# Optimization experiments

Measured on AMD Instinct MI355X. Metric: run time of the kernel, lower is better.

## Reference

```python
import jax, jax.numpy as jnp
import numpy as np

B, T, C = 2, 2048, 2048
H, HKV, D = 16, 4, 128
R = 64  # rope_dim = head_dim * rotary_pct


def setup_inputs() -> dict:
    key = jax.random.key(0)
    ks = jax.random.split(key, 8)
    s = 0.02
    return {
        "x": jax.random.normal(ks[0], (B, T, C), jnp.float32),
        "cos": jnp.cos(jax.random.normal(ks[1], (T, R), jnp.float32)),
        "sin": jnp.sin(jax.random.normal(ks[2], (T, R), jnp.float32)),
        "Wq": jax.random.normal(ks[3], (C, C), jnp.float32) * s,
        "Wk": jax.random.normal(ks[4], (C, HKV * D), jnp.float32) * s,
        "Wv": jax.random.normal(ks[5], (C, HKV * D), jnp.float32) * s,
        "Wo": jax.random.normal(ks[6], (C, C), jnp.float32) * s,
        "gate": jax.random.normal(ks[7], (H,), jnp.float32) * 0.1 - 3.0,
    }


def _rotate_half(t):
    t1, t2 = t[..., : t.shape[-1] // 2], t[..., t.shape[-1] // 2:]
    return jnp.concatenate([-t2, t1], axis=-1)


def reference(x, cos, sin, Wq, Wk, Wv, Wo, gate):
    # projections -> (B, heads, T, D)
    q = (x @ Wq).reshape(B, T, H, D).transpose(0, 2, 1, 3)
    k = (x @ Wk).reshape(B, T, HKV, D).transpose(0, 2, 1, 3)
    v = (x @ Wv).reshape(B, T, HKV, D).transpose(0, 2, 1, 3)

    # partial RoPE on first R dims; cos/sin (T,R) broadcast over (B,h,T,R)
    q_r = q[..., :R] * cos + _rotate_half(q[..., :R]) * sin
    k_r = k[..., :R] * cos + _rotate_half(k[..., :R]) * sin
    q = jnp.concatenate([q_r, q[..., R:]], axis=-1)
    k = jnp.concatenate([k_r, k[..., R:]], axis=-1)

    # GQA: repeat_interleave kv heads to match H
    rep = H // HKV
    k = jnp.repeat(k, rep, axis=1)
    v = jnp.repeat(v, rep, axis=1)

    scale = D ** -0.5
    att = jnp.einsum("bhtd,bhsd->bhts", q, k) * scale  # (B,H,T,T)
    causal = jnp.tril(jnp.ones((T, T), bool))
    att = jnp.where(causal, att, -jnp.inf)
    att = jax.nn.softmax(att, axis=-1)

    # post-softmax learned per-head threshold gate
    thr = jax.nn.sigmoid(gate)[None, :, None, None]
    att = att * (att >= thr).astype(att.dtype)

    y = jnp.einsum("bhts,bhsd->bhtd", att, v)
    y = y.transpose(0, 2, 1, 3).reshape(B, T, C)
    return y @ Wo
```

## Files before the change

kernel.cpp:

```cpp
#include <hip/hip_runtime.h>
#include <stdint.h>

#define Bdim 2
#define Tdim 2048
#define Cdim 2048
#define Hdim 16
#define HKVdim 4
#define KVdim 512
#define KT 32

typedef __attribute__((ext_vector_type(8))) short bf16x8;
typedef __attribute__((ext_vector_type(4))) float f32x4;

#define GLOAD16(gp, lp) __builtin_amdgcn_global_load_lds( \
    (const __attribute__((address_space(1))) void*)(gp),  \
    (__attribute__((address_space(3))) void*)(lp), 16, 0, 0)

__device__ __forceinline__ unsigned short f2bf(float f) {
  union { float f; unsigned u; } a; a.f = f;
  unsigned u = a.u + 0x7FFFu + ((a.u >> 16) & 1u);
  return (unsigned short)(u >> 16);
}
__device__ __forceinline__ float bf2f(unsigned short h) {
  union { float f; unsigned u; } a; a.u = ((unsigned)h) << 16;
  return a.f;
}

__global__ void split_x_kernel(const float* __restrict__ x, unsigned short* __restrict__ hi,
                               unsigned short* __restrict__ lo, int n4) {
  int i = blockIdx.x * blockDim.x + threadIdx.x;
  int stride = gridDim.x * blockDim.x;
  const float4* x4 = (const float4*)x;
  ushort4* h4 = (ushort4*)hi;
  ushort4* l4 = (ushort4*)lo;
  for (; i < n4; i += stride) {
    float4 f = x4[i];
    ushort4 h, l;
    h.x = f2bf(f.x); l.x = f2bf(f.x - bf2f(h.x));
    h.y = f2bf(f.y); l.y = f2bf(f.y - bf2f(h.y));
    h.z = f2bf(f.z); l.z = f2bf(f.z - bf2f(h.z));
    h.w = f2bf(f.w); l.w = f2bf(f.w - bf2f(h.w));
    h4[i] = h; l4[i] = l;
  }
}

__global__ void transpose_split_kernel(const float* __restrict__ in, unsigned short* __restrict__ hi,
                                       unsigned short* __restrict__ lo, int K, int N) {
  __shared__ float tile[32][33];
  int k0 = blockIdx.x * 32, n0 = blockIdx.y * 32;
  int tx = threadIdx.x, ty = threadIdx.y;
#pragma unroll
  for (int i = 0; i < 32; i += 8)
    tile[ty + i][tx] = in[(size_t)(k0 + ty + i) * N + n0 + tx];
  __syncthreads();
#pragma unroll
  for (int i = 0; i < 32; i += 8) {
    float f = tile[tx][ty + i];
    size_t o = (size_t)(n0 + ty + i) * K + k0 + tx;
    unsigned short hb = f2bf(f);
    hi[o] = hb;
    if (lo) lo[o] = f2bf(f - bf2f(hb));
  }
}

__global__ __launch_bounds__(256) void qkv_gemm_kernel(
    const unsigned short* __restrict__ xhi, const unsigned short* __restrict__ xlo,
    const unsigned short* __restrict__ WqThi, const unsigned short* __restrict__ WqTlo,
    const unsigned short* __restrict__ WkThi, const unsigned short* __restrict__ WkTlo,
    const unsigned short* __restrict__ WvThi,
    const float* __restrict__ cs, const float* __restrict__ sn,
    unsigned short* __restrict__ qhi, unsigned short* __restrict__ qlo,
    unsigned short* __restrict__ khi, unsigned short* __restrict__ klo,
    unsigned short* __restrict__ vun)
{
  __shared__ alignas(16) unsigned short sAh[2][128 * 32];
  __shared__ alignas(16) unsigned short sAl[2][128 * 32];
  __shared__ alignas(16) unsigned short sBh[2][128 * 32];
  __shared__ alignas(16) unsigned short sBl[2][128 * 32];
  const int K = 2048;
  int tid = threadIdx.x;
  int wid = tid >> 6, lane = tid & 63;
  int bm = blockIdx.x, bn = blockIdx.y;
  int wr = wid >> 1, wc = wid & 1;
  int ln15 = lane & 15;
  int jsw = (((lane >> 4) ^ ((ln15 >> 1) & 3)) * 8);
  int srow = lane >> 2;
  int scol = (((lane & 3) ^ ((lane >> 3) & 3)) * 8);
  bool three = bn < 20;

  const unsigned short *Bh, *Bl = WqTlo;
  int brow;
  if (bn < 16)      { Bh = WqThi; Bl = WqTlo; brow = bn * 128; }
  else if (bn < 20) { Bh = WkThi; Bl = WkTlo; brow = (bn - 16) * 128; }
  else              { Bh = WvThi;             brow = (bn - 20) * 128; }

  f32x4 acc[4][4];
#pragma unroll
  for (int m = 0; m < 4; ++m)
#pragma unroll
    for (int n = 0; n < 4; ++n)
      acc[m][n] = f32x4{0.f, 0.f, 0.f, 0.f};

  const unsigned short* a0 = xhi + (size_t)(bm * 128 + wid * 32 + srow) * K + scol;
  const unsigned short* a1 = xlo + (size_t)(bm * 128 + wid * 32 + srow) * K + scol;
  const unsigned short* b0 = Bh + (size_t)(brow + wid * 32 + srow) * K + scol;
  const unsigned short* b1 = Bl + (size_t)(brow + wid * 32 + srow) * K + scol;
  int wlds = wid * 32 * 32;

  int nk = K >> 5;
  if (three) {
    auto stage3 = [&](int buf, int kt) {
      const unsigned short* ak = a0 + kt * 32;
      const unsigned short* alk = a1 + kt * 32;
      const unsigned short* bk = b0 + kt * 32;
      const unsigned short* blk = b1 + kt * 32;
      GLOAD16(ak,          &sAh[buf][wlds]);
      GLOAD16(ak + 16 * K, &sAh[buf][wlds + 16 * 32]);
      GLOAD16(alk,          &sAl[buf][wlds]);
      GLOAD16(alk + 16 * K, &sAl[buf][wlds + 16 * 32]);
      GLOAD16(bk,          &sBh[buf][wlds]);
      GLOAD16(bk + 16 * K, &sBh[buf][wlds + 16 * 32]);
      GLOAD16(blk,          &sBl[buf][wlds]);
      GLOAD16(blk + 16 * K, &sBl[buf][wlds + 16 * 32]);
    };
    stage3(0, 0);
    __syncthreads();
    int buf = 0;
    for (int kt = 0; kt < nk; ++kt) {
      bf16x8 afh[4], afl[4], bfh[4], bfl[4];
#pragma unroll
      for (int m = 0; m < 4; ++m) {
        afh[m] = *(const bf16x8*)&sAh[buf][(wr * 64 + m * 16 + ln15) * 32 + jsw];
        afl[m] = *(const bf16x8*)&sAl[buf][(wr * 64 + m * 16 + ln15) * 32 + jsw];
      }
#pragma unroll
      for (int n = 0; n < 4; ++n) {
        bfh[n] = *(const bf16x8*)&sBh[buf][(wc * 64 + n * 16 + ln15) * 32 + jsw];
        bfl[n] = *(const bf16x8*)&sBl[buf][(wc * 64 + n * 16 + ln15) * 32 + jsw];
      }
      if (kt + 1 < nk) stage3(buf ^ 1, kt + 1);
      __builtin_amdgcn_s_setprio(1);
#pragma unroll
      for (int m = 0; m < 4; ++m)
#pragma unroll
        for (int n = 0; n < 4; ++n)
          acc[m][n] = __builtin_amdgcn_mfma_f32_16x16x32_bf16(afh[m], bfh[n], acc[m][n], 0, 0, 0);
#pragma unroll
      for (int m = 0; m < 4; ++m)
#pragma unroll
        for (int n = 0; n < 4; ++n)
          acc[m][n] = __builtin_amdgcn_mfma_f32_16x16x32_bf16(afl[m], bfh[n], acc[m][n], 0, 0, 0);
#pragma unroll
      for (int m = 0; m < 4; ++m)
#pragma unroll
        for (int n = 0; n < 4; ++n)
          acc[m][n] = __builtin_amdgcn_mfma_f32_16x16x32_bf16(afh[m], bfl[n], acc[m][n], 0, 0, 0);
      __builtin_amdgcn_s_setprio(0);
      __syncthreads();
      buf ^= 1;
    }
  } else {
    auto stage1 = [&](int buf, int kt) {
      const unsigned short* ak = a0 + kt * 32;
      const unsigned short* bk = b0 + kt * 32;
      GLOAD16(ak,          &sAh[buf][wlds]);
      GLOAD16(ak + 16 * K, &sAh[buf][wlds + 16 * 32]);
      GLOAD16(bk,          &sBh[buf][wlds]);
      GLOAD16(bk + 16 * K, &sBh[buf][wlds + 16 * 32]);
    };
    stage1(0, 0);
    __syncthreads();
    int buf = 0;
    for (int kt = 0; kt < nk; ++kt) {
      bf16x8 afh[4], bfh[4];
#pragma unroll
      for (int m = 0; m < 4; ++m)
        afh[m] = *(const bf16x8*)&sAh[buf][(wr * 64 + m * 16 + ln15) * 32 + jsw];
#pragma unroll
      for (int n = 0; n < 4; ++n)
        bfh[n] = *(const bf16x8*)&sBh[buf][(wc * 64 + n * 16 + ln15) * 32 + jsw];
      if (kt + 1 < nk) stage1(buf ^ 1, kt + 1);
      __builtin_amdgcn_s_setprio(1);
#pragma unroll
      for (int m = 0; m < 4; ++m)
#pragma unroll
        for (int n = 0; n < 4; ++n)
          acc[m][n] = __builtin_amdgcn_mfma_f32_16x16x32_bf16(afh[m], bfh[n], acc[m][n], 0, 0, 0);
      __builtin_amdgcn_s_setprio(0);
      __syncthreads();
      buf ^= 1;
    }
  }

  int orow0 = bm * 128 + wr * 64 + (lane >> 4) * 4;
  if (bn < 20) {
    int nh = (bn < 16) ? Hdim : HKVdim;
    int h  = (bn < 16) ? bn : bn - 16;
    unsigned short* oph = (bn < 16) ? qhi : khi;
    unsigned short* opl = (bn < 16) ? qlo : klo;
#pragma unroll
    for (int m = 0; m < 4; ++m)
#pragma unroll
      for (int r = 0; r < 4; ++r) {
        int row = orow0 + m * 16 + r;
        int t = row & (Tdim - 1), b = row >> 11;
        size_t obase = (((size_t)(b * nh + h)) * Tdim + t) * 128;
#pragma unroll
        for (int n = 0; n < 4; ++n) {
          int d = wc * 64 + n * 16 + ln15;
          float o;
          if (wc == 0) {
            float c = cs[t * 64 + d], s = sn[t * 64 + d];
            o = (n < 2) ? (acc[m][n][r] * c - acc[m][n + 2][r] * s)
                        : (acc[m][n][r] * c + acc[m][n - 2][r] * s);
          } else o = acc[m][n][r];
          unsigned short hb = f2bf(o);
          oph[obase + d] = hb;
          opl[obase + d] = f2bf(o - bf2f(hb));
        }
      }
  } else {
    int g = bn - 20;
#pragma unroll
    for (int m = 0; m < 4; ++m)
#pragma unroll
      for (int r = 0; r < 4; ++r) {
        int row = orow0 + m * 16 + r;
        int t = row & (Tdim - 1), b = row >> 11;
        size_t obase = (((size_t)(b * HKVdim + g)) * Tdim + t) * 128;
#pragma unroll
        for (int n = 0; n < 4; ++n)
          vun[obase + wc * 64 + n * 16 + ln15] = f2bf(acc[m][n][r]);
      }
  }
}

__global__ __launch_bounds__(256) void gemm_wo_kernel(
    const unsigned short* __restrict__ A, const unsigned short* __restrict__ Bt,
    float* __restrict__ C)
{
  __shared__ alignas(16) unsigned short sA[2][128 * 32];
  __shared__ alignas(16) unsigned short sB[2][128 * 32];
  const int K = 2048, ldc = 2048;
  int tid = threadIdx.x;
  int wid = tid >> 6, lane = tid & 63;
  int bm = blockIdx.x, bn = blockIdx.y;
  int wr = wid >> 1, wc = wid & 1;
  int ln15 = lane & 15;
  int jsw = (((lane >> 4) ^ ((ln15 >> 1) & 3)) * 8);
  int srow = lane >> 2;
  int scol = (((lane & 3) ^ ((lane >> 3) & 3)) * 8);

  f32x4 acc[4][4];
#pragma unroll
  for (int m = 0; m < 4; ++m)
#pragma unroll
    for (int n = 0; n < 4; ++n)
      acc[m][n] = f32x4{0.f, 0.f, 0.f, 0.f};

  const unsigned short* a0 = A + (size_t)(bm * 128 + wid * 32 + srow) * K + scol;
  const unsigned short* b0 = Bt + (size_t)(bn * 128 + wid * 32 + srow) * K + scol;
  int wlds = wid * 32 * 32;

  auto stage = [&](int buf, int kt) {
    const unsigned short* ak = a0 + kt * 32;
    const unsigned short* bk = b0 + kt * 32;
    GLOAD16(ak,          &sA[buf][wlds]);
    GLOAD16(ak + 16 * K, &sA[buf][wlds + 16 * 32]);
    GLOAD16(bk,          &sB[buf][wlds]);
    GLOAD16(bk + 16 * K, &sB[buf][wlds + 16 * 32]);
  };
  int nk = K >> 5;
  stage(0, 0);
  __syncthreads();
  int buf = 0;
  for (int kt = 0; kt < nk; ++kt) {
    bf16x8 af[4], bfv[4];
#pragma unroll
    for (int m = 0; m < 4; ++m)
      af[m] = *(const bf16x8*)&sA[buf][(wr * 64 + m * 16 + ln15) * 32 + jsw];
#pragma unroll
    for (int n = 0; n < 4; ++n)
      bfv[n] = *(const bf16x8*)&sB[buf][(wc * 64 + n * 16 + ln15) * 32 + jsw];
    if (kt + 1 < nk) stage(buf ^ 1, kt + 1);
    __builtin_amdgcn_s_setprio(1);
#pragma unroll
    for (int m = 0; m < 4; ++m)
#pragma unroll
      for (int n = 0; n < 4; ++n)
        acc[m][n] = __builtin_amdgcn_mfma_f32_16x16x32_bf16(af[m], bfv[n], acc[m][n], 0, 0, 0);
    __builtin_amdgcn_s_setprio(0);
    __syncthreads();
    buf ^= 1;
  }

  int orow0 = bm * 128 + wr * 64 + (lane >> 4) * 4;
  int ocol0 = bn * 128 + wc * 64 + ln15;
#pragma unroll
  for (int m = 0; m < 4; ++m)
#pragma unroll
    for (int n = 0; n < 4; ++n)
#pragma unroll
      for (int r = 0; r < 4; ++r)
        C[(size_t)(orow0 + m * 16 + r) * ldc + ocol0 + n * 16] = acc[m][n][r];
}

__global__ void transpose_v_bf16_kernel(const unsigned short* __restrict__ vsrc,
                                        unsigned short* __restrict__ vt) {
  __shared__ unsigned short tile[32][33];
  int bg = blockIdx.x;
  int t0 = blockIdx.y * 32, d0 = blockIdx.z * 32;
  int tx = threadIdx.x, ty = threadIdx.y;
#pragma unroll
  for (int i = 0; i < 32; i += 8)
    tile[ty + i][tx] = vsrc[((size_t)bg * Tdim + t0 + ty + i) * 128 + d0 + tx];
  __syncthreads();
#pragma unroll
  for (int i = 0; i < 32; i += 8)
    vt[((size_t)(bg * 128 + d0 + ty + i)) * Tdim + t0 + tx] = tile[tx][ty + i];
}

__global__ __launch_bounds__(1024, 4) void attn_kernel(
    const unsigned short* __restrict__ qhi, const unsigned short* __restrict__ qlo,
    const unsigned short* __restrict__ khi, const unsigned short* __restrict__ klo,
    const unsigned short* __restrict__ vt, const float* __restrict__ gate,
    unsigned short* __restrict__ y)
{
  __shared__ alignas(16) unsigned short sKh[2][KT * 128];
  __shared__ alignas(16) unsigned short sKl[2][KT * 128];
  __shared__ alignas(16) unsigned short sV[2][128 * KT];
  __shared__ alignas(16) unsigned short sP[16][16 * 40];
  __shared__ float sBM[16][64];

  int qb = (gridDim.x - 1) - blockIdx.x;
  int bh = blockIdx.y;
  int b = bh >> 4, h = bh & 15;
  int g = h >> 2;
  int t0 = qb * 256;
  int tid = threadIdx.x, wid = tid >> 6, lane = tid & 63;
  int ln15 = lane & 15, j16 = (lane >> 4) * 16, ro4 = (lane >> 4) * 4;
  const float cs2 = 0.08838834764831845f * 1.4426950408889634f;
  const float M2  = 8.0f * 1.4426950408889634f;

  const unsigned short* kh_base = khi + (((size_t)b * HKVdim + g) * Tdim) * 128;
  const unsigned short* kl_base = klo + (((size_t)b * HKVdim + g) * Tdim) * 128;
  const unsigned short* v_base  = vt  + (((size_t)b * HKVdim + g) * 128) * (size_t)Tdim;

  bf16x8 aqh[4], aql[4];
  {
    size_t qoff = ((((size_t)b * Hdim + h) * Tdim) + t0 + wid * 16 + ln15) * 128 + (lane >> 4) * 8;
#pragma unroll
    for (int kf = 0; kf < 4; ++kf) {
      aqh[kf] = *(const bf16x8*)(qhi + qoff + kf * 32);
      aql[kf] = *(const bf16x8*)(qlo + qoff + kf * 32);
    }
  }
  float thr = 1.f / (1.f + expf(-gate[h]));

  int nkb = (qb + 1) * 8;
  int tq_lo = t0 + wid * 16;

  auto stageK = [&](int buf, int kb) {
    if (wid < 8) {
      int o = wid * 1024 + lane * 16;
      int row = o >> 8;
      int col = (o & 255) ^ ((row & 7) << 4);
      size_t goff = ((size_t)(kb * KT + row)) * 256 + col;
      GLOAD16((const char*)kh_base + goff, (char*)sKh[buf] + wid * 1024);
      GLOAD16((const char*)kl_base + goff, (char*)sKl[buf] + wid * 1024);
    }
  };
  auto stageV = [&](int buf, int kb) {
    if (wid >= 8) {
      int o = (wid - 8) * 1024 + lane * 16;
      int row = o >> 6;
      int col = (o & 63) ^ (((row ^ (row >> 2)) & 3) << 4);
      size_t goff = (size_t)row * (Tdim * 2) + (size_t)kb * 64 + col;
      GLOAD16((const char*)v_base + goff, (char*)sV[buf] + (wid - 8) * 1024);
    }
  };
  auto qk = [&](int buf, f32x4* s) {
    __builtin_amdgcn_s_setprio(1);
#pragma unroll
    for (int nf = 0; nf < 2; ++nf) {
      f32x4 a = {0.f, 0.f, 0.f, 0.f};
      int krow = nf * 16 + ln15;
      int sw = (krow & 7) << 4;
#pragma unroll
      for (int kf = 0; kf < 4; ++kf) {
        int boff = (kf * 64 + j16) ^ sw;
        bf16x8 bh_ = *(const bf16x8*)((const char*)sKh[buf] + krow * 256 + boff);
        bf16x8 bl_ = *(const bf16x8*)((const char*)sKl[buf] + krow * 256 + boff);
        a = __builtin_amdgcn_mfma_f32_16x16x32_bf16(aqh[kf], bh_, a, 0, 0, 0);
        a = __builtin_amdgcn_mfma_f32_16x16x32_bf16(aql[kf], bh_, a, 0, 0, 0);
        a = __builtin_amdgcn_mfma_f32_16x16x32_bf16(aqh[kf], bl_, a, 0, 0, 0);
      }
      s[nf] = a;
    }
    __builtin_amdgcn_s_setprio(0);
  };

  float lloc[4];
#pragma unroll
  for (int r = 0; r < 4; ++r) lloc[r] = 0.f;

  stageK(0, 0);
  __syncthreads();
  for (int kb = 0; kb < nkb; ++kb) {
    int buf = kb & 1;
    if (kb + 1 < nkb) stageK(buf ^ 1, kb + 1);
    if (kb * KT <= tq_lo + 15) {
      f32x4 s[2];
      qk(buf, s);
      float wmax = -1e30f;
      bool full = (kb * KT + KT - 1) <= tq_lo;
      if (full) {
#pragma unroll
        for (int nf = 0; nf < 2; ++nf)
#pragma unroll
          for (int r = 0; r < 4; ++r) {
            float v = s[nf][r] * cs2;
            wmax = fmaxf(wmax, v);
            lloc[r] += __builtin_exp2f(v - M2);
          }
      } else {
#pragma unroll
        for (int nf = 0; nf < 2; ++nf) {
          int tk = kb * KT + nf * 16 + ln15;
#pragma unroll
          for (int r = 0; r < 4; ++r) {
            int tq = tq_lo + ro4 + r;
            float v = (tk <= tq) ? s[nf][r] * cs2 : -1e30f;
            wmax = fmaxf(wmax, v);
            lloc[r] += __builtin_exp2f(v - M2);
          }
        }
      }
#pragma unroll
      for (int off = 1; off < 64; off <<= 1)
        wmax = fmaxf(wmax, __shfl_xor(wmax, off));
      if (lane == 0) sBM[wid][kb] = wmax;
    }
    __syncthreads();
  }

  float lrow[4], lgate2[4];
#pragma unroll
  for (int r = 0; r < 4; ++r) {
    float l = lloc[r];
#pragma unroll
    for (int off = 1; off < 16; off <<= 1) l += __shfl_xor(l, off);
    lrow[r] = l;
    lgate2[r] = __log2f(thr * l) + M2;
  }
  float lgmin = fminf(fminf(lgate2[0], lgate2[1]), fminf(lgate2[2], lgate2[3]));
  lgmin = fminf(lgmin, __shfl_xor(lgmin, 16));
  lgmin = fminf(lgmin, __shfl_xor(lgmin, 32));

  f32x4 yacc[8];
#pragma unroll
  for (int n = 0; n < 8; ++n) yacc[n] = f32x4{0.f, 0.f, 0.f, 0.f};

  stageK(0, 0);
  stageV(0, 0);
  __syncthreads();
  for (int kb = 0; kb < nkb; ++kb) {
    int buf = kb & 1;
    if (kb + 1 < nkb) { stageK(buf ^ 1, kb + 1); stageV(buf ^ 1, kb + 1); }
    if (kb * KT <= tq_lo + 15 && sBM[wid][kb] >= lgmin) {
      f32x4 s[2];
      qk(buf, s);
      bool anyk = false;
      float pv[2][4];
      bool full = (kb * KT + KT - 1) <= tq_lo;
#pragma unroll
      for (int nf = 0; nf < 2; ++nf) {
        int tk = kb * KT + nf * 16 + ln15;
#pragma unroll
        for (int r = 0; r < 4; ++r) {
          int tq = tq_lo + ro4 + r;
          float v = s[nf][r] * cs2;
          bool keep = (full || tk <= tq) && (v >= lgate2[r]);
          float p = 0.f;
          if (keep) { p = __builtin_exp2f(v - M2); anyk = true; }
          pv[nf][r] = p;
        }
      }
      if (__any(anyk)) {
#pragma unroll
        for (int nf = 0; nf < 2; ++nf)
#pragma unroll
          for (int r = 0; r < 4; ++r)
            sP[wid][(ro4 + r) * 40 + nf * 16 + ln15] = f2bf(pv[nf][r]);
        __builtin_amdgcn_s_setprio(1);
        bf16x8 pa = *(const bf16x8*)&sP[wid][ln15 * 40 + (lane >> 4) * 8];
#pragma unroll
        for (int nf2 = 0; nf2 < 8; ++nf2) {
          int vrow = nf2 * 16 + ln15;
          int vboff = j16 ^ (((vrow ^ (vrow >> 2)) & 3) << 4);
          bf16x8 vb = *(const bf16x8*)((const char*)sV[buf] + vrow * 64 + vboff);
          yacc[nf2] = __builtin_amdgcn_mfma_f32_16x16x32_bf16(pa, vb, yacc[nf2], 0, 0, 0);
        }
        __builtin_amdgcn_s_setprio(0);
      }
    }
    __syncthreads();
  }

#pragma unroll
  for (int r = 0; r < 4; ++r) {
    int tq = t0 + wid * 16 + ro4 + r;
    float invl = 1.f / lrow[r];
    size_t base = ((size_t)(b * Tdim + tq)) * Cdim + h * 128;
#pragma unroll
    for (int nf2 = 0; nf2 < 8; ++nf2)
      y[base + nf2 * 16 + ln15] = f2bf(yacc[nf2][r] * invl);
  }
}

extern "C" void kernel_launch(void* const* d_in, const int* in_sizes, int n_in,
                              void* d_out, int out_size, void* d_ws, size_t ws_size,
                              hipStream_t stream)
{
  (void)in_sizes; (void)n_in; (void)out_size; (void)ws_size;
  const float* x    = (const float*)d_in[0];
  const float* cosT = (const float*)d_in[1];
  const float* sinT = (const float*)d_in[2];
  const float* Wq   = (const float*)d_in[3];
  const float* Wk   = (const float*)d_in[4];
  const float* Wv   = (const float*)d_in[5];
  const float* Wo   = (const float*)d_in[6];
  const float* gate = (const float*)d_in[7];
  float* out = (float*)d_out;

  char* ws = (char*)d_ws;
  size_t off = 0;
  auto alloc = [&](size_t bytes) -> char* {
    char* p = ws + off; off += (bytes + 255) & ~(size_t)255; return p;
  };
  const size_t NX = (size_t)Bdim * Tdim * Cdim;
  const size_t NK = (size_t)Bdim * Tdim * KVdim;

  unsigned short* xhi   = (unsigned short*)alloc(NX * 2);
  unsigned short* xlo   = (unsigned short*)alloc(NX * 2);
  unsigned short* WqThi = (unsigned short*)alloc((size_t)Cdim * Cdim * 2);
  unsigned short* WqTlo = (unsigned short*)alloc((size_t)Cdim * Cdim * 2);
  unsigned short* WkThi = (unsigned short*)alloc((size_t)Cdim * KVdim * 2);
  unsigned short* WkTlo = (unsigned short*)alloc((size_t)Cdim * KVdim * 2);
  unsigned short* WvThi = (unsigned short*)alloc((size_t)Cdim * KVdim * 2);
  unsigned short* WoThi = (unsigned short*)alloc((size_t)Cdim * Cdim * 2);
  unsigned short* qhi   = (unsigned short*)alloc(NX * 2);
  unsigned short* qlo   = (unsigned short*)alloc(NX * 2);
  unsigned short* khi   = (unsigned short*)alloc(NK * 2);
  unsigned short* klo   = (unsigned short*)alloc(NK * 2);
  unsigned short* vun   = (unsigned short*)alloc(NK * 2);
  unsigned short* vtr   = (unsigned short*)alloc(NK * 2);
  unsigned short* yb    = (unsigned short*)alloc(NX * 2);

  dim3 tb(32, 8);
  split_x_kernel<<<2048, 256, 0, stream>>>(x, xhi, xlo, (int)(NX >> 2));
  transpose_split_kernel<<<dim3(64, 64), tb, 0, stream>>>(Wq, WqThi, WqTlo, Cdim, Cdim);
  transpose_split_kernel<<<dim3(64, 16), tb, 0, stream>>>(Wk, WkThi, WkTlo, Cdim, KVdim);
  transpose_split_kernel<<<dim3(64, 16), tb, 0, stream>>>(Wv, WvThi, nullptr, Cdim, KVdim);
  transpose_split_kernel<<<dim3(64, 64), tb, 0, stream>>>(Wo, WoThi, nullptr, Cdim, Cdim);

  qkv_gemm_kernel<<<dim3(32, 24), 256, 0, stream>>>(
      xhi, xlo, WqThi, WqTlo, WkThi, WkTlo, WvThi,
      cosT, sinT, qhi, qlo, khi, klo, vun);
  transpose_v_bf16_kernel<<<dim3(8, 64, 4), tb, 0, stream>>>(vun, vtr);

  attn_kernel<<<dim3(8, 32), 1024, 0, stream>>>(qhi, qlo, khi, klo, vtr, gate, yb);

  gemm_wo_kernel<<<dim3(32, 16), 256, 0, stream>>>(yb, WoThi, out);
}
```

Measured before the change: 393.7 us.

## Use atomic work queue for QKV GEMM and halve attention block size

The QKV GEMM becomes a persistent kernel of 512 blocks that pull tile indices from a global atomic counter. The costlier three-pass Q and K tiles are handed out first and the cheaper single-pass V tiles last, to balance load across CUs. The attention kernel moves from 1024-thread blocks covering 256 query rows to 512-thread blocks covering 128 rows, which doubles the grid. It now single-buffers V, issuing the V load for the current key block at the start of each iteration and waiting on vmcnt just before the PV MFMAs. The trade-offs are atomic and barrier overhead per GEMM item, and V load latency that is now less hidden in attention.

```diff
diff --git a/kernel.cpp b/kernel.cpp
--- a/kernel.cpp
+++ b/kernel.cpp
@@ -15,6 +15,7 @@
 #define GLOAD16(gp, lp) __builtin_amdgcn_global_load_lds( \
     (const __attribute__((address_space(1))) void*)(gp),  \
     (__attribute__((address_space(3))) void*)(lp), 16, 0, 0)
+#define WAITV(N) asm volatile("s_waitcnt vmcnt(" #N ")" ::: "memory")
 
 __device__ __forceinline__ unsigned short f2bf(float f) {
   union { float f; unsigned u; } a; a.f = f;
@@ -71,167 +72,180 @@
     const float* __restrict__ cs, const float* __restrict__ sn,
     unsigned short* __restrict__ qhi, unsigned short* __restrict__ qlo,
     unsigned short* __restrict__ khi, unsigned short* __restrict__ klo,
-    unsigned short* __restrict__ vun)
+    unsigned short* __restrict__ vun, unsigned* __restrict__ qcnt)
 {
   __shared__ alignas(16) unsigned short sAh[2][128 * 32];
   __shared__ alignas(16) unsigned short sAl[2][128 * 32];
   __shared__ alignas(16) unsigned short sBh[2][128 * 32];
   __shared__ alignas(16) unsigned short sBl[2][128 * 32];
+  __shared__ int s_item;
   const int K = 2048;
   int tid = threadIdx.x;
   int wid = tid >> 6, lane = tid & 63;
-  int bm = blockIdx.x, bn = blockIdx.y;
   int wr = wid >> 1, wc = wid & 1;
   int ln15 = lane & 15;
   int jsw = (((lane >> 4) ^ ((ln15 >> 1) & 3)) * 8);
   int srow = lane >> 2;
   int scol = (((lane & 3) ^ ((lane >> 3) & 3)) * 8);
-  bool three = bn < 20;
-
-  const unsigned short *Bh, *Bl = WqTlo;
-  int brow;
-  if (bn < 16)      { Bh = WqThi; Bl = WqTlo; brow = bn * 128; }
-  else if (bn < 20) { Bh = WkThi; Bl = WkTlo; brow = (bn - 16) * 128; }
-  else              { Bh = WvThi;             brow = (bn - 20) * 128; }
-
-  f32x4 acc[4][4];
-#pragma unroll
-  for (int m = 0; m < 4; ++m)
-#pragma unroll
-    for (int n = 0; n < 4; ++n)
-      acc[m][n] = f32x4{0.f, 0.f, 0.f, 0.f};
-
-  const unsigned short* a0 = xhi + (size_t)(bm * 128 + wid * 32 + srow) * K + scol;
-  const unsigned short* a1 = xlo + (size_t)(bm * 128 + wid * 32 + srow) * K + scol;
-  const unsigned short* b0 = Bh + (size_t)(brow + wid * 32 + srow) * K + scol;
-  const unsigned short* b1 = Bl + (size_t)(brow + wid * 32 + srow) * K + scol;
   int wlds = wid * 32 * 32;
-
   int nk = K >> 5;
-  if (three) {
-    auto stage3 = [&](int buf, int kt) {
-      const unsigned short* ak = a0 + kt * 32;
-      const unsigned short* alk = a1 + kt * 32;
-      const unsigned short* bk = b0 + kt * 32;
-      const unsigned short* blk = b1 + kt * 32;
-      GLOAD16(ak,          &sAh[buf][wlds]);
-      GLOAD16(ak + 16 * K, &sAh[buf][wlds + 16 * 32]);
-      GLOAD16(alk,          &sAl[buf][wlds]);
-      GLOAD16(alk + 16 * K, &sAl[buf][wlds + 16 * 32]);
-      GLOAD16(bk,          &sBh[buf][wlds]);
-      GLOAD16(bk + 16 * K, &sBh[buf][wlds + 16 * 32]);
-      GLOAD16(blk,          &sBl[buf][wlds]);
-      GLOAD16(blk + 16 * K, &sBl[buf][wlds + 16 * 32]);
-    };
-    stage3(0, 0);
+
+  for (;;) {
     __syncthreads();
-    int buf = 0;
-    for (int kt = 0; kt < nk; ++kt) {
-      bf16x8 afh[4], afl[4], bfh[4], bfl[4];
-#pragma unroll
-      for (int m = 0; m < 4; ++m) {
-        afh[m] = *(const bf16x8*)&sAh[buf][(wr * 64 + m * 16 + ln15) * 32 + jsw];
-        afl[m] = *(const bf16x8*)&sAl[buf][(wr * 64 + m * 16 + ln15) * 32 + jsw];
+    if (tid == 0) s_item = (int)atomicAdd(qcnt, 1u);
+    __syncthreads();
+    int item = s_item;
+    if (item >= 768) break;
+
+    int bm, bn;
+    if (item < 512)      { bm = item >> 4; bn = item & 15; }
+    else if (item < 640) { int i = item - 512; bm = i >> 2; bn = 16 + (i & 3); }
+    else                 { int i = item - 640; bm = i >> 2; bn = 20 + (i & 3); }
+    bool three = bn < 20;
+
+    const unsigned short *Bh, *Bl = WqTlo;
+    int brow;
+    if (bn < 16)      { Bh = WqThi; Bl = WqTlo; brow = bn * 128; }
+    else if (bn < 20) { Bh = WkThi; Bl = WkTlo; brow = (bn - 16) * 128; }
+    else              { Bh = WvThi;             brow = (bn - 20) * 128; }
+
+    f32x4 acc[4][4];
+#pragma unroll
+    for (int m = 0; m < 4; ++m)
+#pragma unroll
+      for (int n = 0; n < 4; ++n)
+        acc[m][n] = f32x4{0.f, 0.f, 0.f, 0.f};
+
+    const unsigned short* a0 = xhi + (size_t)(bm * 128 + wid * 32 + srow) * K + scol;
+    const unsigned short* a1 = xlo + (size_t)(bm * 128 + wid * 32 + srow) * K + scol;
+    const unsigned short* b0 = Bh + (size_t)(brow + wid * 32 + srow) * K + scol;
+    const unsigned short* b1 = Bl + (size_t)(brow + wid * 32 + srow) * K + scol;
+
+    if (three) {
+      auto stage3 = [&](int buf, int kt) {
+        const unsigned short* ak = a0 + kt * 32;
+        const unsigned short* alk = a1 + kt * 32;
+        const unsigned short* bk = b0 + kt * 32;
+        const unsigned short* blk = b1 + kt * 32;
+        GLOAD16(ak,          &sAh[buf][wlds]);
+        GLOAD16(ak + 16 * K, &sAh[buf][wlds + 16 * 32]);
+        GLOAD16(alk,          &sAl[buf][wlds]);
+        GLOAD16(alk + 16 * K, &sAl[buf][wlds + 16 * 32]);
+        GLOAD16(bk,          &sBh[buf][wlds]);
+        GLOAD16(bk + 16 * K, &sBh[buf][wlds + 16 * 32]);
+        GLOAD16(blk,          &sBl[buf][wlds]);
+        GLOAD16(blk + 16 * K, &sBl[buf][wlds + 16 * 32]);
+      };
+      stage3(0, 0);
+      __syncthreads();
+      int buf = 0;
+      for (int kt = 0; kt < nk; ++kt) {
+        bf16x8 afh[4], afl[4], bfh[4], bfl[4];
+#pragma unroll
+        for (int m = 0; m < 4; ++m) {
+          afh[m] = *(const bf16x8*)&sAh[buf][(wr * 64 + m * 16 + ln15) * 32 + jsw];
+          afl[m] = *(const bf16x8*)&sAl[buf][(wr * 64 + m * 16 + ln15) * 32 + jsw];
+        }
+#pragma unroll
+        for (int n = 0; n < 4; ++n) {
+          bfh[n] = *(const bf16x8*)&sBh[buf][(wc * 64 + n * 16 + ln15) * 32 + jsw];
+          bfl[n] = *(const bf16x8*)&sBl[buf][(wc * 64 + n * 16 + ln15) * 32 + jsw];
+        }
+        if (kt + 1 < nk) stage3(buf ^ 1, kt + 1);
+        __builtin_amdgcn_s_setprio(1);
+#pragma unroll
+        for (int m = 0; m < 4; ++m)
+#pragma unroll
+          for (int n = 0; n < 4; ++n)
+            acc[m][n] = __builtin_amdgcn_mfma_f32_16x16x32_bf16(afh[m], bfh[n], acc[m][n], 0, 0, 0);
+#pragma unroll
+        for (int m = 0; m < 4; ++m)
+#pragma unroll
+          for (int n = 0; n < 4; ++n)
+            acc[m][n] = __builtin_amdgcn_mfma_f32_16x16x32_bf16(afl[m], bfh[n], acc[m][n], 0, 0, 0);
+#pragma unroll
+        for (int m = 0; m < 4; ++m)
+#pragma unroll
+          for (int n = 0; n < 4; ++n)
+            acc[m][n] = __builtin_amdgcn_mfma_f32_16x16x32_bf16(afh[m], bfl[n], acc[m][n], 0, 0, 0);
+        __builtin_amdgcn_s_setprio(0);
+        __syncthreads();
+        buf ^= 1;
       }
-#pragma unroll
-      for (int n = 0; n < 4; ++n) {
-        bfh[n] = *(const bf16x8*)&sBh[buf][(wc * 64 + n * 16 + ln15) * 32 + jsw];
-        bfl[n] = *(const bf16x8*)&sBl[buf][(wc * 64 + n * 16 + ln15) * 32 + jsw];
+    } else {
+      auto stage1 = [&](int buf, int kt) {
+        const unsigned short* ak = a0 + kt * 32;
+        const unsigned short* bk = b0 + kt * 32;
+        GLOAD16(ak,          &sAh[buf][wlds]);
+        GLOAD16(ak + 16 * K, &sAh[buf][wlds + 16 * 32]);
+        GLOAD16(bk,          &sBh[buf][wlds]);
+        GLOAD16(bk + 16 * K, &sBh[buf][wlds + 16 * 32]);
+      };
+      stage1(0, 0);
+      __syncthreads();
+      int buf = 0;
+      for (int kt = 0; kt < nk; ++kt) {
+        bf16x8 afh[4], bfh[4];
+#pragma unroll
+        for (int m = 0; m < 4; ++m)
+          afh[m] = *(const bf16x8*)&sAh[buf][(wr * 64 + m * 16 + ln15) * 32 + jsw];
+#pragma unroll
+        for (int n = 0; n < 4; ++n)
+          bfh[n] = *(const bf16x8*)&sBh[buf][(wc * 64 + n * 16 + ln15) * 32 + jsw];
+        if (kt + 1 < nk) stage1(buf ^ 1, kt + 1);
+        __builtin_amdgcn_s_setprio(1);
+#pragma unroll
+        for (int m = 0; m < 4; ++m)
+#pragma unroll
+          for (int n = 0; n < 4; ++n)
+            acc[m][n] = __builtin_amdgcn_mfma_f32_16x16x32_bf16(afh[m], bfh[n], acc[m][n], 0, 0, 0);
+        __builtin_amdgcn_s_setprio(0);
+        __syncthreads();
+        buf ^= 1;
       }
-      if (kt + 1 < nk) stage3(buf ^ 1, kt + 1);
-      __builtin_amdgcn_s_setprio(1);
+    }
+
+    int orow0 = bm * 128 + wr * 64 + (lane >> 4) * 4;
+    if (bn < 20) {
+      int nh = (bn < 16) ? Hdim : HKVdim;
+      int h  = (bn < 16) ? bn : bn - 16;
+      unsigned short* oph = (bn < 16) ? qhi : khi;
+      unsigned short* opl = (bn < 16) ? qlo : klo;
 #pragma unroll
       for (int m = 0; m < 4; ++m)
 #pragma unroll
-        for (int n = 0; n < 4; ++n)
-          acc[m][n] = __builtin_amdgcn_mfma_f32_16x16x32_bf16(afh[m], bfh[n], acc[m][n], 0, 0, 0);
+        for (int r = 0; r < 4; ++r) {
+          int row = orow0 + m * 16 + r;
+          int t = row & (Tdim - 1), b = row >> 11;
+          size_t obase = (((size_t)(b * nh + h)) * Tdim + t) * 128;
+#pragma unroll
+          for (int n = 0; n < 4; ++n) {
+            int d = wc * 64 + n * 16 + ln15;
+            float o;
+            if (wc == 0) {
+              float c = cs[t * 64 + d], s = sn[t * 64 + d];
+              o = (n < 2) ? (acc[m][n][r] * c - acc[m][n + 2][r] * s)
+                          : (acc[m][n][r] * c + acc[m][n - 2][r] * s);
+            } else o = acc[m][n][r];
+            unsigned short hb = f2bf(o);
+            oph[obase + d] = hb;
+            opl[obase + d] = f2bf(o - bf2f(hb));
+          }
+        }
+    } else {
+      int g = bn - 20;
 #pragma unroll
       for (int m = 0; m < 4; ++m)
 #pragma unroll
-        for (int n = 0; n < 4; ++n)
-          acc[m][n] = __builtin_amdgcn_mfma_f32_16x16x32_bf16(afl[m], bfh[n], acc[m][n], 0, 0, 0);
-#pragma unroll
-      for (int m = 0; m < 4; ++m)
-#pragma unroll
-        for (int n = 0; n < 4; ++n)
-          acc[m][n] = __builtin_amdgcn_mfma_f32_16x16x32_bf16(afh[m], bfl[n], acc[m][n], 0, 0, 0);
-      __builtin_amdgcn_s_setprio(0);
-      __syncthreads();
-      buf ^= 1;
+        for (int r = 0; r < 4; ++r) {
+          int row = orow0 + m * 16 + r;
+          int t = row & (Tdim - 1), b = row >> 11;
+          size_t obase = (((size_t)(b * HKVdim + g)) * Tdim + t) * 128;
+#pragma unroll
+          for (int n = 0; n < 4; ++n)
+            vun[obase + wc * 64 + n * 16 + ln15] = f2bf(acc[m][n][r]);
+        }
     }
-  } else {
-    auto stage1 = [&](int buf, int kt) {
-      const unsigned short* ak = a0 + kt * 32;
-      const unsigned short* bk = b0 + kt * 32;
-      GLOAD16(ak,          &sAh[buf][wlds]);
-      GLOAD16(ak + 16 * K, &sAh[buf][wlds + 16 * 32]);
-      GLOAD16(bk,          &sBh[buf][wlds]);
-      GLOAD16(bk + 16 * K, &sBh[buf][wlds + 16 * 32]);
-    };
-    stage1(0, 0);
-    __syncthreads();
-    int buf = 0;
-    for (int kt = 0; kt < nk; ++kt) {
-      bf16x8 afh[4], bfh[4];
-#pragma unroll
-      for (int m = 0; m < 4; ++m)
-        afh[m] = *(const bf16x8*)&sAh[buf][(wr * 64 + m * 16 + ln15) * 32 + jsw];
-#pragma unroll
-      for (int n = 0; n < 4; ++n)
-        bfh[n] = *(const bf16x8*)&sBh[buf][(wc * 64 + n * 16 + ln15) * 32 + jsw];
-      if (kt + 1 < nk) stage1(buf ^ 1, kt + 1);
-      __builtin_amdgcn_s_setprio(1);
-#pragma unroll
-      for (int m = 0; m < 4; ++m)
-#pragma unroll
-        for (int n = 0; n < 4; ++n)
-          acc[m][n] = __builtin_amdgcn_mfma_f32_16x16x32_bf16(afh[m], bfh[n], acc[m][n], 0, 0, 0);
-      __builtin_amdgcn_s_setprio(0);
-      __syncthreads();
-      buf ^= 1;
-    }
-  }
-
-  int orow0 = bm * 128 + wr * 64 + (lane >> 4) * 4;
-  if (bn < 20) {
-    int nh = (bn < 16) ? Hdim : HKVdim;
-    int h  = (bn < 16) ? bn : bn - 16;
-    unsigned short* oph = (bn < 16) ? qhi : khi;
-    unsigned short* opl = (bn < 16) ? qlo : klo;
-#pragma unroll
-    for (int m = 0; m < 4; ++m)
-#pragma unroll
-      for (int r = 0; r < 4; ++r) {
-        int row = orow0 + m * 16 + r;
-        int t = row & (Tdim - 1), b = row >> 11;
-        size_t obase = (((size_t)(b * nh + h)) * Tdim + t) * 128;
-#pragma unroll
-        for (int n = 0; n < 4; ++n) {
-          int d = wc * 64 + n * 16 + ln15;
-          float o;
-          if (wc == 0) {
-            float c = cs[t * 64 + d], s = sn[t * 64 + d];
-            o = (n < 2) ? (acc[m][n][r] * c - acc[m][n + 2][r] * s)
-                        : (acc[m][n][r] * c + acc[m][n - 2][r] * s);
-          } else o = acc[m][n][r];
-          unsigned short hb = f2bf(o);
-          oph[obase + d] = hb;
-          opl[obase + d] = f2bf(o - bf2f(hb));
-        }
-      }
-  } else {
-    int g = bn - 20;
-#pragma unroll
-    for (int m = 0; m < 4; ++m)
-#pragma unroll
-      for (int r = 0; r < 4; ++r) {
-        int row = orow0 + m * 16 + r;
-        int t = row & (Tdim - 1), b = row >> 11;
-        size_t obase = (((size_t)(b * HKVdim + g)) * Tdim + t) * 128;
-#pragma unroll
-        for (int n = 0; n < 4; ++n)
-          vun[obase + wc * 64 + n * 16 + ln15] = f2bf(acc[m][n][r]);
-      }
   }
 }
 
@@ -320,7 +334,7 @@
     vt[((size_t)(bg * 128 + d0 + ty + i)) * Tdim + t0 + tx] = tile[tx][ty + i];
 }
 
-__global__ __launch_bounds__(1024, 4) void attn_kernel(
+__global__ __launch_bounds__(512, 6) void attn_kernel(
     const unsigned short* __restrict__ qhi, const unsigned short* __restrict__ qlo,
     const unsigned short* __restrict__ khi, const unsigned short* __restrict__ klo,
     const unsigned short* __restrict__ vt, const float* __restrict__ gate,
@@ -328,15 +342,15 @@
 {
   __shared__ alignas(16) unsigned short sKh[2][KT * 128];
   __shared__ alignas(16) unsigned short sKl[2][KT * 128];
-  __shared__ alignas(16) unsigned short sV[2][128 * KT];
-  __shared__ alignas(16) unsigned short sP[16][16 * 40];
-  __shared__ float sBM[16][64];
+  __shared__ alignas(16) unsigned short sV[128 * KT];
+  __shared__ alignas(16) unsigned short sP[8][16 * 40];
+  __shared__ float sBM[8][64];
 
   int qb = (gridDim.x - 1) - blockIdx.x;
   int bh = blockIdx.y;
   int b = bh >> 4, h = bh & 15;
   int g = h >> 2;
-  int t0 = qb * 256;
+  int t0 = qb * 128;
   int tid = threadIdx.x, wid = tid >> 6, lane = tid & 63;
   int ln15 = lane & 15, j16 = (lane >> 4) * 16, ro4 = (lane >> 4) * 4;
   const float cs2 = 0.08838834764831845f * 1.4426950408889634f;
@@ -357,27 +371,23 @@
   }
   float thr = 1.f / (1.f + expf(-gate[h]));
 
-  int nkb = (qb + 1) * 8;
+  int nkb = (qb + 1) * 4;
   int tq_lo = t0 + wid * 16;
 
   auto stageK = [&](int buf, int kb) {
-    if (wid < 8) {
-      int o = wid * 1024 + lane * 16;
-      int row = o >> 8;
-      int col = (o & 255) ^ ((row & 7) << 4);
-      size_t goff = ((size_t)(kb * KT + row)) * 256 + col;
-      GLOAD16((const char*)kh_base + goff, (char*)sKh[buf] + wid * 1024);
-      GLOAD16((const char*)kl_base + goff, (char*)sKl[buf] + wid * 1024);
-    }
+    int o = wid * 1024 + lane * 16;
+    int row = o >> 8;
+    int col = (o & 255) ^ ((row & 7) << 4);
+    size_t goff = ((size_t)(kb * KT + row)) * 256 + col;
+    GLOAD16((const char*)kh_base + goff, (char*)sKh[buf] + wid * 1024);
+    GLOAD16((const char*)kl_base + goff, (char*)sKl[buf] + wid * 1024);
   };
-  auto stageV = [&](int buf, int kb) {
-    if (wid >= 8) {
-      int o = (wid - 8) * 1024 + lane * 16;
-      int row = o >> 6;
-      int col = (o & 63) ^ (((row ^ (row >> 2)) & 3) << 4);
-      size_t goff = (size_t)row * (Tdim * 2) + (size_t)kb * 64 + col;
-      GLOAD16((const char*)v_base + goff, (char*)sV[buf] + (wid - 8) * 1024);
-    }
+  auto stageV = [&](int kb) {
+    int o = wid * 1024 + lane * 16;
+    int row = o >> 6;
+    int col = (o & 63) ^ (((row ^ (row >> 2)) & 3) << 4);
+    size_t goff = (size_t)row * (Tdim * 2) + (size_t)kb * 64 + col;
+    GLOAD16((const char*)v_base + goff, (char*)sV + wid * 1024);
   };
   auto qk = [&](int buf, f32x4* s) {
     __builtin_amdgcn_s_setprio(1);
@@ -462,11 +472,11 @@
   for (int n = 0; n < 8; ++n) yacc[n] = f32x4{0.f, 0.f, 0.f, 0.f};
 
   stageK(0, 0);
-  stageV(0, 0);
   __syncthreads();
   for (int kb = 0; kb < nkb; ++kb) {
     int buf = kb & 1;
-    if (kb + 1 < nkb) { stageK(buf ^ 1, kb + 1); stageV(buf ^ 1, kb + 1); }
+    stageV(kb);
+    if (kb + 1 < nkb) stageK(buf ^ 1, kb + 1);
     if (kb * KT <= tq_lo + 15 && sBM[wid][kb] >= lgmin) {
       f32x4 s[2];
       qk(buf, s);
@@ -492,13 +502,14 @@
 #pragma unroll
           for (int r = 0; r < 4; ++r)
             sP[wid][(ro4 + r) * 40 + nf * 16 + ln15] = f2bf(pv[nf][r]);
+        if (kb + 1 < nkb) { WAITV(2); } else { WAITV(0); }
         __builtin_amdgcn_s_setprio(1);
         bf16x8 pa = *(const bf16x8*)&sP[wid][ln15 * 40 + (lane >> 4) * 8];
 #pragma unroll
         for (int nf2 = 0; nf2 < 8; ++nf2) {
           int vrow = nf2 * 16 + ln15;
           int vboff = j16 ^ (((vrow ^ (vrow >> 2)) & 3) << 4);
-          bf16x8 vb = *(const bf16x8*)((const char*)sV[buf] + vrow * 64 + vboff);
+          bf16x8 vb = *(const bf16x8*)((const char*)sV + vrow * 64 + vboff);
           yacc[nf2] = __builtin_amdgcn_mfma_f32_16x16x32_bf16(pa, vb, yacc[nf2], 0, 0, 0);
         }
         __builtin_amdgcn_s_setprio(0);
@@ -556,6 +567,9 @@
   unsigned short* vun   = (unsigned short*)alloc(NK * 2);
   unsigned short* vtr   = (unsigned short*)alloc(NK * 2);
   unsigned short* yb    = (unsigned short*)alloc(NX * 2);
+  unsigned*       qcnt  = (unsigned*)alloc(256);
+
+  hipMemsetAsync(qcnt, 0, 4, stream);
 
   dim3 tb(32, 8);
   split_x_kernel<<<2048, 256, 0, stream>>>(x, xhi, xlo, (int)(NX >> 2));
@@ -564,12 +578,12 @@
   transpose_split_kernel<<<dim3(64, 16), tb, 0, stream>>>(Wv, WvThi, nullptr, Cdim, KVdim);
   transpose_split_kernel<<<dim3(64, 64), tb, 0, stream>>>(Wo, WoThi, nullptr, Cdim, Cdim);
 
-  qkv_gemm_kernel<<<dim3(32, 24), 256, 0, stream>>>(
+  qkv_gemm_kernel<<<512, 256, 0, stream>>>(
       xhi, xlo, WqThi, WqTlo, WkThi, WkTlo, WvThi,
-      cosT, sinT, qhi, qlo, khi, klo, vun);
+      cosT, sinT, qhi, qlo, khi, klo, vun, qcnt);
   transpose_v_bf16_kernel<<<dim3(8, 64, 4), tb, 0, stream>>>(vun, vtr);
 
-  attn_kernel<<<dim3(8, 32), 1024, 0, stream>>>(qhi, qlo, khi, klo, vtr, gate, yb);
+  attn_kernel<<<dim3(16, 32), 512, 0, stream>>>(qhi, qlo, khi, klo, vtr, gate, yb);
 
   gemm_wo_kernel<<<dim3(32, 16), 256, 0, stream>>>(yb, WoThi, out);
 }
```

Result: slower. 472.8 us (+20.1%).
